# Kernel tuning notes

Hardware: AMD Instinct MI355X
Metric: run time of the kernel (lower is better)

The kernel has to match this reference:

```python
import jax, jax.numpy as jnp
import numpy as np

D_MODEL = 1024
N_HEADS = 16
D_HEAD = D_MODEL // N_HEADS
D_FF = 4 * D_MODEL
EPS = 1e-5


def _layernorm(x, g, b):
    mu = jnp.mean(x, axis=-1, keepdims=True)
    var = jnp.var(x, axis=-1, keepdims=True)
    return (x - mu) * jax.lax.rsqrt(var + EPS) * g + b


def setup_inputs() -> dict:
    key = jax.random.key(0)
    ks = jax.random.split(key, 16)
    s_attn = 1.0 / np.sqrt(D_MODEL)
    s_ff1 = 1.0 / np.sqrt(D_MODEL)
    s_ff2 = 1.0 / np.sqrt(D_FF)
    inp = {
        'x': jax.random.normal(ks[0], (2, 2048, D_MODEL), dtype=jnp.float32),
        'Wq': jax.random.uniform(ks[1], (D_MODEL, D_MODEL), jnp.float32, -s_attn, s_attn),
        'bq': jax.random.uniform(ks[2], (D_MODEL,), jnp.float32, -s_attn, s_attn),
        'Wk': jax.random.uniform(ks[3], (D_MODEL, D_MODEL), jnp.float32, -s_attn, s_attn),
        'bk': jax.random.uniform(ks[4], (D_MODEL,), jnp.float32, -s_attn, s_attn),
        'Wv': jax.random.uniform(ks[5], (D_MODEL, D_MODEL), jnp.float32, -s_attn, s_attn),
        'bv': jax.random.uniform(ks[6], (D_MODEL,), jnp.float32, -s_attn, s_attn),
        'Wo': jax.random.uniform(ks[7], (D_MODEL, D_MODEL), jnp.float32, -s_attn, s_attn),
        'bo': jax.random.uniform(ks[8], (D_MODEL,), jnp.float32, -s_attn, s_attn),
        'W1': jax.random.uniform(ks[9], (D_MODEL, D_FF), jnp.float32, -s_ff1, s_ff1),
        'b1': jax.random.uniform(ks[10], (D_FF,), jnp.float32, -s_ff1, s_ff1),
        'W2': jax.random.uniform(ks[11], (D_FF, D_MODEL), jnp.float32, -s_ff2, s_ff2),
        'b2': jax.random.uniform(ks[12], (D_MODEL,), jnp.float32, -s_ff2, s_ff2),
        'ln1_g': jnp.ones((D_MODEL,), jnp.float32),
        'ln1_b': jnp.zeros((D_MODEL,), jnp.float32),
        'ln2_g': jnp.ones((D_MODEL,), jnp.float32),
        'ln2_b': jnp.zeros((D_MODEL,), jnp.float32),
    }
    return inp


def reference(x, Wq, bq, Wk, bk, Wv, bv, Wo, bo, W1, b1, W2, b2, ln1_g, ln1_b, ln2_g, ln2_b):
    B, T, D = x.shape
    scale = D_HEAD ** -0.5

    # pre-norm MHSA + residual
    h = _layernorm(x, ln1_g, ln1_b)
    def split(z):  # [B,T,D] -> [B,H,T,d_h]
        return z.reshape(B, T, N_HEADS, D_HEAD).transpose(0, 2, 1, 3)
    Q = split(h @ Wq + bq)
    K = split(h @ Wk + bk)
    V = split(h @ Wv + bv)
    scores = jnp.einsum('bhqd,bhkd->bhqk', Q, K) * scale  # [B,H,T,T]
    attn = jax.nn.softmax(scores, axis=-1)
    out = jnp.einsum('bhqk,bhkd->bhqd', attn, V)
    out = out.transpose(0, 2, 1, 3).reshape(B, T, D)
    x = x + (out @ Wo + bo)

    # pre-norm FFN + residual
    h = _layernorm(x, ln2_g, ln2_b)
    ff = jax.nn.gelu(h @ W1 + b1, approximate=False) @ W2 + b2
    return x + ff
```

## Files before the change

### kernel.cpp

```cpp
#include <hip/hip_runtime.h>
#include <math.h>

#define SEQ   2048
#define DM    1024
#define LDQKV 3072
#define MTOK  4096

typedef float  f32x4   __attribute__((ext_vector_type(4)));
typedef __bf16 bf16x8  __attribute__((ext_vector_type(8)));
typedef short  short8  __attribute__((ext_vector_type(8)));
typedef short  short4v __attribute__((ext_vector_type(4)));

__device__ __forceinline__ short f2bf(float f) {
  union { float f; unsigned u; } v; v.f = f;
  unsigned r = v.u + 0x7fffu + ((v.u >> 16) & 1u);
  return (short)(r >> 16);
}

__device__ __forceinline__ void gl_lds16(const void* g, void* l) {
  __builtin_amdgcn_global_load_lds(
      (const __attribute__((address_space(1))) void*)g,
      (__attribute__((address_space(3))) void*)l, 16, 0, 0);
}

__device__ __forceinline__ f32x4 mfma_bf16(bf16x8 a, bf16x8 b, f32x4 c) {
  return __builtin_amdgcn_mfma_f32_16x16x32_bf16(a, b, c, 0, 0, 0);
}

__global__ __launch_bounds__(256) void transpose_cast_k(
    const float* __restrict__ W, short* __restrict__ Wt, int K, int N)
{
  __shared__ float tile[32][33];
  const int n0 = blockIdx.x * 32, k0 = blockIdx.y * 32;
  const int tx = threadIdx.x & 31, ty = threadIdx.x >> 5;
#pragma unroll
  for (int i = 0; i < 4; i++)
    tile[ty + i * 8][tx] = W[(size_t)(k0 + ty + i * 8) * N + n0 + tx];
  __syncthreads();
#pragma unroll
  for (int i = 0; i < 4; i++)
    Wt[(size_t)(n0 + ty + i * 8) * K + k0 + tx] = f2bf(tile[tx][ty + i * 8]);
}

__global__ __launch_bounds__(256) void ln_k(
    const float* __restrict__ x, const float* __restrict__ g,
    const float* __restrict__ b, short* __restrict__ out)
{
  const int row = blockIdx.x;
  const int tid = threadIdx.x;
  const float4 v = ((const float4*)(x + (size_t)row * DM))[tid];
  float s  = v.x + v.y + v.z + v.w;
  float ss = v.x * v.x + v.y * v.y + v.z * v.z + v.w * v.w;
#pragma unroll
  for (int m = 32; m >= 1; m >>= 1) { s += __shfl_xor(s, m); ss += __shfl_xor(ss, m); }
  __shared__ float red[8];
  const int wid = tid >> 6;
  if ((tid & 63) == 0) { red[wid] = s; red[4 + wid] = ss; }
  __syncthreads();
  s  = red[0] + red[1] + red[2] + red[3];
  ss = red[4] + red[5] + red[6] + red[7];
  const float mu  = s * (1.f / DM);
  const float var = ss * (1.f / DM) - mu * mu;
  const float rs  = rsqrtf(var + 1e-5f);
  const float4 gv = ((const float4*)g)[tid];
  const float4 bv = ((const float4*)b)[tid];
  short4v o;
  o[0] = f2bf((v.x - mu) * rs * gv.x + bv.x);
  o[1] = f2bf((v.y - mu) * rs * gv.y + bv.y);
  o[2] = f2bf((v.z - mu) * rs * gv.z + bv.z);
  o[3] = f2bf((v.w - mu) * rs * gv.w + bv.w);
  *(short4v*)(out + (size_t)row * DM + tid * 4) = o;
}

__global__ __launch_bounds__(256) void concat_bias_k(
    const float* __restrict__ bq, const float* __restrict__ bk,
    const float* __restrict__ bv, float* __restrict__ o)
{
  int i = blockIdx.x * 256 + threadIdx.x;
  if (i < 3072) {
    float v = (i < 1024) ? bq[i] : (i < 2048 ? bk[i - 1024] : bv[i - 2048]);
    o[i] = v;
  }
}

__global__ __launch_bounds__(256) void vtrans_k(
    const short* __restrict__ V, short* __restrict__ Vt)
{
  const int b = blockIdx.z, h = blockIdx.y, t0 = blockIdx.x * 64;
  __shared__ short tile[64][72];
  const int tid = threadIdx.x;
  const int r = tid >> 2, c = (tid & 3) * 16;
  const short* src = V + (size_t)(b * SEQ + t0 + r) * LDQKV + h * 64 + c;
  *(short8*)&tile[r][c]     = *(const short8*)src;
  *(short8*)&tile[r][c + 8] = *(const short8*)(src + 8);
  __syncthreads();
  const int d = tid >> 2;
  short8 o0, o1;
#pragma unroll
  for (int k = 0; k < 8; k++) o0[k] = tile[c + k][d];
#pragma unroll
  for (int k = 0; k < 8; k++) o1[k] = tile[c + 8 + k][d];
  short* dst = Vt + (((size_t)(b * 16 + h) * 64) + d) * 2048 + t0 + c;
  *(short8*)dst       = o0;
  *(short8*)(dst + 8) = o1;
}

template <bool GELU_, bool RESID, bool OUTBF16>
__global__ __launch_bounds__(512) void gemm256(
    const short* __restrict__ A, const short* __restrict__ Bt,
    const float* __restrict__ bias, const float* __restrict__ resid,
    void* __restrict__ Cout, int M, int N, int K)
{
  __shared__ __align__(16) short Atile[2][256 * 64];
  __shared__ __align__(16) short Btile[2][256 * 64];

  const int tid = threadIdx.x, lane = tid & 63, wid = tid >> 6;
  const int wm = wid >> 2, wn = wid & 3;

  const int nbn = N >> 8;
  const int chunk = gridDim.x >> 3;
  const int swz = (blockIdx.x & 7) * chunk + (blockIdx.x >> 3);
  const int bm = (swz / nbn) * 256;
  const int bn = (swz % nbn) * 256;

  f32x4 acc[8][4] = {};

  const int srow  = wid * 8 + (lane >> 3);
  const int sslot = (lane & 7) ^ ((lane >> 3) & 7);
  const short* Asrc = A  + (size_t)(bm + srow) * K + sslot * 8;
  const short* Bsrc = Bt + (size_t)(bn + srow) * K + sslot * 8;

#define STAGE256(buf, k0)                                                     \
  {                                                                           \
    _Pragma("unroll")                                                         \
    for (int j = 0; j < 4; j++) {                                             \
      gl_lds16(Asrc + (size_t)(j * 64) * K + (k0), &Atile[buf][(j * 64 + wid * 8) * 64]); \
      gl_lds16(Bsrc + (size_t)(j * 64) * K + (k0), &Btile[buf][(j * 64 + wid * 8) * 64]); \
    }                                                                         \
  }

  const int aRowBase = (wm * 128 + (lane & 15)) * 128;
  const int bRowBase = (wn * 64  + (lane & 15)) * 128;
  const int slot0 = (((lane >> 4)    ) ^ (lane & 7)) * 16;
  const int slot1 = (((lane >> 4) + 4) ^ (lane & 7)) * 16;

#define COMPUTE256(buf)                                                       \
  {                                                                           \
    const char* Ab_ = (const char*)&Atile[buf][0];                            \
    const char* Bb_ = (const char*)&Btile[buf][0];                            \
    _Pragma("unroll")                                                         \
    for (int ks = 0; ks < 2; ks++) {                                          \
      const int sl = ks ? slot1 : slot0;                                      \
      bf16x8 a[8], b[4];                                                      \
      _Pragma("unroll")                                                       \
      for (int mi = 0; mi < 8; mi++)                                          \
        a[mi] = *(const bf16x8*)(Ab_ + aRowBase + mi * 2048 + sl);            \
      _Pragma("unroll")                                                       \
      for (int ni = 0; ni < 4; ni++)                                          \
        b[ni] = *(const bf16x8*)(Bb_ + bRowBase + ni * 2048 + sl);            \
      __builtin_amdgcn_s_setprio(1);                                          \
      _Pragma("unroll")                                                       \
      for (int mi = 0; mi < 8; mi++)                                          \
        _Pragma("unroll")                                                     \
        for (int ni = 0; ni < 4; ni++)                                        \
          acc[mi][ni] = mfma_bf16(a[mi], b[ni], acc[mi][ni]);                 \
      __builtin_amdgcn_s_setprio(0);                                          \
    }                                                                         \
  }

  STAGE256(0, 0);
  __syncthreads();

  int cur = 0;
  const int ntiles = K >> 6;
  for (int t = 1; t < ntiles; ++t) {
    STAGE256(cur ^ 1, t * 64);
    COMPUTE256(cur);
    __syncthreads();
    cur ^= 1;
  }
  COMPUTE256(cur);

#pragma unroll
  for (int mi = 0; mi < 8; mi++) {
#pragma unroll
    for (int ni = 0; ni < 4; ni++) {
      const int col = bn + wn * 64 + ni * 16 + (lane & 15);
      const float bs = bias[col];
#pragma unroll
      for (int j = 0; j < 4; j++) {
        const int row = bm + wm * 128 + mi * 16 + (lane >> 4) * 4 + j;
        float v = acc[mi][ni][j] + bs;
        if (GELU_) v = 0.5f * v * (1.0f + erff(v * 0.70710678118654752f));
        if (RESID) v += resid[(size_t)row * N + col];
        if (OUTBF16) ((short*)Cout)[(size_t)row * N + col] = f2bf(v);
        else         ((float*)Cout)[(size_t)row * N + col] = v;
      }
    }
  }
#undef STAGE256
#undef COMPUTE256
}

template <bool GELU_, bool RESID, bool OUTBF16>
__global__ __launch_bounds__(256) void gemm_bt(
    const short* __restrict__ A, const short* __restrict__ Bt,
    const float* __restrict__ bias, const float* __restrict__ resid,
    void* __restrict__ Cout, int M, int N, int K)
{
  __shared__ __align__(16) short Abuf[2][128 * 32];
  __shared__ __align__(16) short Bbuf[2][128 * 32];
  const int tid = threadIdx.x, lane = tid & 63, wid = tid >> 6;
  const int wr = wid >> 1, wc = wid & 1;
  const int bm = blockIdx.x * 128, bn = blockIdx.y * 128;

  f32x4 acc[4][4] = {};

  const int arow  = wid * 32 + (lane >> 2);
  const int acol8 = ((lane & 3) ^ ((lane >> 2) & 3)) * 8;
  const short* Ag0 = A  + (size_t)(bm + arow)      * K + acol8;
  const short* Ag1 = A  + (size_t)(bm + arow + 16) * K + acol8;
  const short* Bg0 = Bt + (size_t)(bn + arow)      * K + acol8;
  const short* Bg1 = Bt + (size_t)(bn + arow + 16) * K + acol8;

  const int l0 = (wid * 32) * 32, l1 = (wid * 32 + 16) * 32;
  const int rslot = ((lane >> 4) ^ (lane & 3)) * 8;

  gl_lds16(Ag0, &Abuf[0][l0]);
  gl_lds16(Ag1, &Abuf[0][l1]);
  gl_lds16(Bg0, &Bbuf[0][l0]);
  gl_lds16(Bg1, &Bbuf[0][l1]);
  __syncthreads();

  int cur = 0;
  for (int k0 = 32; k0 < K; k0 += 32) {
    const int nxt = cur ^ 1;
    gl_lds16(Ag0 + k0, &Abuf[nxt][l0]);
    gl_lds16(Ag1 + k0, &Abuf[nxt][l1]);
    gl_lds16(Bg0 + k0, &Bbuf[nxt][l0]);
    gl_lds16(Bg1 + k0, &Bbuf[nxt][l1]);

    bf16x8 a[4], b[4];
#pragma unroll
    for (int mi = 0; mi < 4; mi++)
      a[mi] = *(const bf16x8*)&Abuf[cur][(wr * 64 + mi * 16 + (lane & 15)) * 32 + rslot];
#pragma unroll
    for (int ni = 0; ni < 4; ni++)
      b[ni] = *(const bf16x8*)&Bbuf[cur][(wc * 64 + ni * 16 + (lane & 15)) * 32 + rslot];
#pragma unroll
    for (int mi = 0; mi < 4; mi++)
#pragma unroll
      for (int ni = 0; ni < 4; ni++)
        acc[mi][ni] = mfma_bf16(a[mi], b[ni], acc[mi][ni]);

    __syncthreads();
    cur = nxt;
  }

  {
    bf16x8 a[4], b[4];
#pragma unroll
    for (int mi = 0; mi < 4; mi++)
      a[mi] = *(const bf16x8*)&Abuf[cur][(wr * 64 + mi * 16 + (lane & 15)) * 32 + rslot];
#pragma unroll
    for (int ni = 0; ni < 4; ni++)
      b[ni] = *(const bf16x8*)&Bbuf[cur][(wc * 64 + ni * 16 + (lane & 15)) * 32 + rslot];
#pragma unroll
    for (int mi = 0; mi < 4; mi++)
#pragma unroll
      for (int ni = 0; ni < 4; ni++)
        acc[mi][ni] = mfma_bf16(a[mi], b[ni], acc[mi][ni]);
  }

#pragma unroll
  for (int mi = 0; mi < 4; mi++) {
#pragma unroll
    for (int ni = 0; ni < 4; ni++) {
      const int col = bn + wc * 64 + ni * 16 + (lane & 15);
      const float bs = bias[col];
#pragma unroll
      for (int j = 0; j < 4; j++) {
        const int row = bm + wr * 64 + mi * 16 + (lane >> 4) * 4 + j;
        float v = acc[mi][ni][j] + bs;
        if (GELU_) v = 0.5f * v * (1.0f + erff(v * 0.70710678118654752f));
        if (RESID) v += resid[(size_t)row * N + col];
        if (OUTBF16) ((short*)Cout)[(size_t)row * N + col] = f2bf(v);
        else         ((float*)Cout)[(size_t)row * N + col] = v;
      }
    }
  }
}

template <bool GELU_, bool RESID, bool OUTBF16>
__global__ __launch_bounds__(512) void gemm_bt8(
    const short* __restrict__ A, const short* __restrict__ Bt,
    const float* __restrict__ bias, const float* __restrict__ resid,
    void* __restrict__ Cout, int M, int N, int K)
{
  __shared__ __align__(16) short Ab[2][2][128 * 32];
  __shared__ __align__(16) short Bb[2][2][64 * 32];
  const int tid = threadIdx.x, lane = tid & 63, wid = tid >> 6;
  const int kg = wid >> 2, w2 = wid & 3;
  const int wr = w2 >> 1, wc = w2 & 1;
  const int bm = blockIdx.x * 128, bn = blockIdx.y * 64;

  f32x4 acc[4][2] = {};

  const int r_l = lane >> 2;
  const int c8  = ((lane & 3) ^ ((lane >> 2) & 3)) * 8;
  const short* Ag0 = A  + (size_t)(bm + w2 * 32 + r_l)      * K + c8;
  const short* Ag1 = A  + (size_t)(bm + w2 * 32 + 16 + r_l) * K + c8;
  const short* Bg0 = Bt + (size_t)(bn + w2 * 16 + r_l)      * K + c8;

  const int la0 = (w2 * 32) * 32, la1 = (w2 * 32 + 16) * 32, lb0 = (w2 * 16) * 32;
  const int kbase = kg * 32;
  const int rslot = ((lane >> 4) ^ (lane & 3)) * 8;

  gl_lds16(Ag0 + kbase, &Ab[kg][0][la0]);
  gl_lds16(Ag1 + kbase, &Ab[kg][0][la1]);
  gl_lds16(Bg0 + kbase, &Bb[kg][0][lb0]);
  __syncthreads();

  const int nsteps = K >> 6;
  int cur = 0;
  for (int i = 1; i < nsteps; ++i) {
    const int k0 = i * 64 + kbase;
    const int nxt = cur ^ 1;
    gl_lds16(Ag0 + k0, &Ab[kg][nxt][la0]);
    gl_lds16(Ag1 + k0, &Ab[kg][nxt][la1]);
    gl_lds16(Bg0 + k0, &Bb[kg][nxt][lb0]);

    bf16x8 a[4], b[2];
#pragma unroll
    for (int mi = 0; mi < 4; mi++)
      a[mi] = *(const bf16x8*)&Ab[kg][cur][(wr * 64 + mi * 16 + (lane & 15)) * 32 + rslot];
#pragma unroll
    for (int ni = 0; ni < 2; ni++)
      b[ni] = *(const bf16x8*)&Bb[kg][cur][(wc * 32 + ni * 16 + (lane & 15)) * 32 + rslot];
#pragma unroll
    for (int mi = 0; mi < 4; mi++)
#pragma unroll
      for (int ni = 0; ni < 2; ni++)
        acc[mi][ni] = mfma_bf16(a[mi], b[ni], acc[mi][ni]);

    __syncthreads();
    cur = nxt;
  }

  {
    bf16x8 a[4], b[2];
#pragma unroll
    for (int mi = 0; mi < 4; mi++)
      a[mi] = *(const bf16x8*)&Ab[kg][cur][(wr * 64 + mi * 16 + (lane & 15)) * 32 + rslot];
#pragma unroll
    for (int ni = 0; ni < 2; ni++)
      b[ni] = *(const bf16x8*)&Bb[kg][cur][(wc * 32 + ni * 16 + (lane & 15)) * 32 + rslot];
#pragma unroll
    for (int mi = 0; mi < 4; mi++)
#pragma unroll
      for (int ni = 0; ni < 2; ni++)
        acc[mi][ni] = mfma_bf16(a[mi], b[ni], acc[mi][ni]);
  }

  __syncthreads();

  float* red = (float*)&Ab[0][0][0];
  const int slot = (w2 * 64 + lane) * 8;
  if (kg == 1) {
#pragma unroll
    for (int mi = 0; mi < 4; mi++)
#pragma unroll
      for (int ni = 0; ni < 2; ni++)
        *(f32x4*)&red[(slot + mi * 2 + ni) * 4] = acc[mi][ni];
  }
  __syncthreads();
  if (kg == 0) {
#pragma unroll
    for (int mi = 0; mi < 4; mi++)
#pragma unroll
      for (int ni = 0; ni < 2; ni++)
        acc[mi][ni] += *(const f32x4*)&red[(slot + mi * 2 + ni) * 4];

#pragma unroll
    for (int mi = 0; mi < 4; mi++) {
#pragma unroll
      for (int ni = 0; ni < 2; ni++) {
        const int col = bn + wc * 32 + ni * 16 + (lane & 15);
        const float bs = bias[col];
#pragma unroll
        for (int j = 0; j < 4; j++) {
          const int row = bm + wr * 64 + mi * 16 + (lane >> 4) * 4 + j;
          float v = acc[mi][ni][j] + bs;
          if (GELU_) v = 0.5f * v * (1.0f + erff(v * 0.70710678118654752f));
          if (RESID) v += resid[(size_t)row * N + col];
          if (OUTBF16) ((short*)Cout)[(size_t)row * N + col] = f2bf(v);
          else         ((float*)Cout)[(size_t)row * N + col] = v;
        }
      }
    }
  }
}

__global__ __launch_bounds__(512, 4) void attn_k(
    const short* __restrict__ Qg, const short* __restrict__ Kg,
    const short* __restrict__ Vt, short* __restrict__ Og)
{
  const int phys = blockIdx.x;
  const int lg = (phys & 7) * 64 + (phys >> 3);
  const int q0 = (lg & 15) * 128;
  const int h  = (lg >> 4) & 15;
  const int b  = lg >> 8;

  const int tid = threadIdx.x, lane = tid & 63, w = tid >> 6;
  const int qlane = lane & 15, g = lane >> 4;

  __shared__ __align__(16) short Kl[2][128 * 64];
  __shared__ __align__(16) short Vl[2][64 * 128];

  const size_t qrow = (size_t)(b * SEQ + q0 + w * 16 + qlane) * LDQKV + h * 64;
  const bf16x8 qf0 = *(const bf16x8*)&Qg[qrow + g * 8];
  const bf16x8 qf1 = *(const bf16x8*)&Qg[qrow + 32 + g * 8];

  const int kslot = (lane & 7) ^ ((lane >> 3) & 7);
  const short* Kg_a[2];
#pragma unroll
  for (int i = 0; i < 2; i++) {
    const int r  = i * 64 + w * 8 + (lane >> 3);
    const int kc = r >> 4, gr = (r >> 2) & 3, jr = r & 3;
    const int a  = 32 * (kc & 3) + 8 * gr + 4 * (kc >> 2) + jr;
    Kg_a[i] = Kg + ((size_t)(b * SEQ) + a) * LDQKV + h * 64 + kslot * 8;
  }
  const short* Vg_s[2];
#pragma unroll
  for (int i = 0; i < 2; i++) {
    const int d  = i * 32 + w * 4 + (lane >> 4);
    const int vs = (lane & 15) ^ (d & 15);
    Vg_s[i] = Vt + ((size_t)(b * 16 + h) * 64 + d) * 2048 + vs * 8;
  }

  float m_run = -1e30f, l_run = 0.f;
  f32x4 oacc[4] = {};
  const float C = 0.125f * 1.44269504088896f;

#pragma unroll
  for (int i = 0; i < 2; i++) {
    gl_lds16(Kg_a[i], &Kl[0][(i * 64 + w * 8) * 64]);
    gl_lds16(Vg_s[i], &Vl[0][(i * 32 + w * 4) * 128]);
  }
  __syncthreads();

  int cur = 0;
  for (int kt = 0; kt < SEQ; kt += 128) {
    const int nxt = cur ^ 1;
    if (kt + 128 < SEQ) {
#pragma unroll
      for (int i = 0; i < 2; i++) {
        gl_lds16(Kg_a[i] + (size_t)(kt + 128) * LDQKV, &Kl[nxt][(i * 64 + w * 8) * 64]);
        gl_lds16(Vg_s[i] + (kt + 128),                 &Vl[nxt][(i * 32 + w * 4) * 128]);
      }
    }
    const char* KbC = (const char*)&Kl[cur][0];
    const char* VbC = (const char*)&Vl[cur][0];

    f32x4 s[8];
#pragma unroll
    for (int kc = 0; kc < 8; kc++) {
      const int kr = kc * 16 + qlane;
      const char* kp = KbC + kr * 128;
      const int sw = (kr & 7) << 4;
      bf16x8 kf0 = *(const bf16x8*)(kp + ((g * 16) ^ sw));
      bf16x8 kf1 = *(const bf16x8*)(kp + ((64 + g * 16) ^ sw));
      f32x4 z = {};
      z = mfma_bf16(kf0, qf0, z);
      z = mfma_bf16(kf1, qf1, z);
      s[kc] = z;
    }

    f32x4 m4 = s[0];
#pragma unroll
    for (int kc = 1; kc < 8; kc++) {
      m4[0] = fmaxf(m4[0], s[kc][0]); m4[1] = fmaxf(m4[1], s[kc][1]);
      m4[2] = fmaxf(m4[2], s[kc][2]); m4[3] = fmaxf(m4[3], s[kc][3]);
    }
    float mt = fmaxf(fmaxf(m4[0], m4[1]), fmaxf(m4[2], m4[3]));
    mt = fmaxf(mt, __shfl_xor(mt, 16));
    mt = fmaxf(mt, __shfl_xor(mt, 32));

    if (!__all(mt - m_run <= 40.0f)) {
      const float mnew = fmaxf(m_run, mt);
      const float r = exp2f((m_run - mnew) * C);
      m_run = mnew;
      l_run *= r;
#pragma unroll
      for (int j = 0; j < 4; j++) {
        const float rj = __shfl(r, g * 4 + j);
#pragma unroll
        for (int dt = 0; dt < 4; dt++) oacc[dt][j] *= rj;
      }
    }

    const float nmc = -m_run * C;
    float rs = 0.f;
    unsigned pw[4][4];
#pragma unroll
    for (int kc = 0; kc < 8; kc++) {
      f32x4 p;
#pragma unroll
      for (int j = 0; j < 4; j++) p[j] = exp2f(fmaf(s[kc][j], C, nmc));
      rs += (p[0] + p[1]) + (p[2] + p[3]);
      unsigned w0, w1;
      asm("v_cvt_pk_bf16_f32 %0, %1, %2" : "=v"(w0) : "v"(p[0]), "v"(p[1]));
      asm("v_cvt_pk_bf16_f32 %0, %1, %2" : "=v"(w1) : "v"(p[2]), "v"(p[3]));
      pw[kc & 3][2 * (kc >> 2) + 0] = w0;
      pw[kc & 3][2 * (kc >> 2) + 1] = w1;
    }
    rs += __shfl_xor(rs, 16);
    rs += __shfl_xor(rs, 32);
    l_run += rs;

#pragma unroll
    for (int ks = 0; ks < 4; ks++) {
      union { unsigned u[4]; bf16x8 v; } pf;
      pf.u[0] = pw[ks][0]; pf.u[1] = pw[ks][1];
      pf.u[2] = pw[ks][2]; pf.u[3] = pw[ks][3];
#pragma unroll
      for (int dt = 0; dt < 4; dt++) {
        const int vr = dt * 16 + qlane;
        bf16x8 vf = *(const bf16x8*)(VbC + vr * 256 + ((64 * ks + 16 * g) ^ ((vr & 15) << 4)));
        oacc[dt] = mfma_bf16(pf.v, vf, oacc[dt]);
      }
    }

    __syncthreads();
    cur = nxt;
  }

  const float linv = 1.f / l_run;
#pragma unroll
  for (int j = 0; j < 4; j++) {
    const float lj = __shfl(linv, g * 4 + j);
    const int tok = q0 + w * 16 + g * 4 + j;
#pragma unroll
    for (int dt = 0; dt < 4; dt++)
      Og[(size_t)(b * SEQ + tok) * DM + h * 64 + dt * 16 + qlane] = f2bf(oacc[dt][j] * lj);
  }
}

extern "C" void kernel_launch(void* const* d_in, const int* in_sizes, int n_in,
                              void* d_out, int out_size, void* d_ws, size_t ws_size,
                              hipStream_t stream)
{
  const float* x    = (const float*)d_in[0];
  const float* Wq   = (const float*)d_in[1];
  const float* bq   = (const float*)d_in[2];
  const float* Wk   = (const float*)d_in[3];
  const float* bk   = (const float*)d_in[4];
  const float* Wv   = (const float*)d_in[5];
  const float* bv   = (const float*)d_in[6];
  const float* Wo   = (const float*)d_in[7];
  const float* bo   = (const float*)d_in[8];
  const float* W1   = (const float*)d_in[9];
  const float* b1   = (const float*)d_in[10];
  const float* W2   = (const float*)d_in[11];
  const float* b2   = (const float*)d_in[12];
  const float* ln1g = (const float*)d_in[13];
  const float* ln1b = (const float*)d_in[14];
  const float* ln2g = (const float*)d_in[15];
  const float* ln2b = (const float*)d_in[16];

  char* ws = (char*)d_ws;
  const size_t MB = 1024 * 1024;
  short* Wqkvt = (short*)(ws + 0 * MB);
  short* Wqt   = Wqkvt;
  short* Wkt   = (short*)(ws + 2 * MB);
  short* Wvt   = (short*)(ws + 4 * MB);
  short* Wot   = (short*)(ws + 6 * MB);
  short* W1t   = (short*)(ws + 8 * MB);
  short* W2t   = (short*)(ws + 16 * MB);
  short* hbuf  = (short*)(ws + 24 * MB);
  short* QKV   = (short*)(ws + 32 * MB);
  short* AO    = (short*)(ws + 56 * MB);
  float* x1    = (float*)(ws + 64 * MB);
  short* Vtb   = (short*)(ws + 64 * MB);
  float* bqkv  = (float*)(ws + 80 * MB);
  short* gbuf  = (short*)(ws + 32 * MB);

  dim3 tb(256);

  transpose_cast_k<<<dim3(32, 32),  tb, 0, stream>>>(Wq, Wqt, 1024, 1024);
  transpose_cast_k<<<dim3(32, 32),  tb, 0, stream>>>(Wk, Wkt, 1024, 1024);
  transpose_cast_k<<<dim3(32, 32),  tb, 0, stream>>>(Wv, Wvt, 1024, 1024);
  transpose_cast_k<<<dim3(32, 32),  tb, 0, stream>>>(Wo, Wot, 1024, 1024);
  transpose_cast_k<<<dim3(128, 32), tb, 0, stream>>>(W1, W1t, 1024, 4096);
  transpose_cast_k<<<dim3(32, 128), tb, 0, stream>>>(W2, W2t, 4096, 1024);
  concat_bias_k<<<dim3(12), tb, 0, stream>>>(bq, bk, bv, bqkv);

  ln_k<<<dim3(MTOK), tb, 0, stream>>>(x, ln1g, ln1b, hbuf);

  gemm_bt<false, false, true><<<dim3(32, 24), tb, 0, stream>>>(
      hbuf, Wqkvt, bqkv, nullptr, QKV, MTOK, 3072, 1024);

  vtrans_k<<<dim3(32, 16, 2), tb, 0, stream>>>(QKV + 2048, Vtb);

  attn_k<<<dim3(512), dim3(512), 0, stream>>>(QKV, QKV + 1024, Vtb, AO);

  gemm_bt8<false, true, false><<<dim3(32, 16), dim3(512), 0, stream>>>(
      AO, Wot, bo, x, x1, MTOK, 1024, 1024);

  ln_k<<<dim3(MTOK), tb, 0, stream>>>(x1, ln2g, ln2b, hbuf);

  gemm256<true, false, true><<<dim3(256), dim3(512), 0, stream>>>(
      hbuf, W1t, b1, nullptr, gbuf, MTOK, 4096, 1024);

  gemm_bt8<false, true, false><<<dim3(32, 16), dim3(512), 0, stream>>>(
      gbuf, W2t, b2, x1, (float*)d_out, MTOK, 1024, 4096);
}
```

Measured before the change: 275.1 us.

## Vectorize weight transpose-cast with 64x64 tiles and use 256-tile GEMM for QKV

Replaces the 32x32 scalar weight transpose/cast kernel with a 64x64 tile version that does float4 loads and 16-byte bf16 stores. It also switches the QKV projection from the 128x128-tile gemm_bt kernel to the larger-tile 512-thread gemm256 kernel already used for FFN1, and deletes gemm_bt. The goal is fewer memory transactions in the per-call weight conversion and more operand reuse in the QKV GEMM. The trade-off is that 192 blocks may underfill the CUs, and the tile reads with stride 65 may hit LDS bank conflicts.

Result: no change. 272.4 us (-1.0%).

```diff
diff --git a/kernel.cpp b/kernel.cpp
--- a/kernel.cpp
+++ b/kernel.cpp
@@ -27,19 +27,30 @@
   return __builtin_amdgcn_mfma_f32_16x16x32_bf16(a, b, c, 0, 0, 0);
 }
 
-__global__ __launch_bounds__(256) void transpose_cast_k(
+__global__ __launch_bounds__(256) void transpose_cast64_k(
     const float* __restrict__ W, short* __restrict__ Wt, int K, int N)
 {
-  __shared__ float tile[32][33];
-  const int n0 = blockIdx.x * 32, k0 = blockIdx.y * 32;
-  const int tx = threadIdx.x & 31, ty = threadIdx.x >> 5;
-#pragma unroll
-  for (int i = 0; i < 4; i++)
-    tile[ty + i * 8][tx] = W[(size_t)(k0 + ty + i * 8) * N + n0 + tx];
-  __syncthreads();
-#pragma unroll
-  for (int i = 0; i < 4; i++)
-    Wt[(size_t)(n0 + ty + i * 8) * K + k0 + tx] = f2bf(tile[tx][ty + i * 8]);
+  __shared__ float tile[64][65];
+  const int n0 = blockIdx.x * 64, k0 = blockIdx.y * 64;
+  const int tid = threadIdx.x;
+  const int lr = tid >> 4, lc = (tid & 15) * 4;
+#pragma unroll
+  for (int i = 0; i < 4; i++) {
+    const float4 v = *(const float4*)&W[(size_t)(k0 + lr + i * 16) * N + n0 + lc];
+    tile[lr + i * 16][lc]     = v.x;
+    tile[lr + i * 16][lc + 1] = v.y;
+    tile[lr + i * 16][lc + 2] = v.z;
+    tile[lr + i * 16][lc + 3] = v.w;
+  }
+  __syncthreads();
+  const int nr = tid >> 3, ks = (tid & 7) * 8;
+#pragma unroll
+  for (int i = 0; i < 2; i++) {
+    short8 o;
+#pragma unroll
+    for (int j = 0; j < 8; j++) o[j] = f2bf(tile[ks + j][nr + i * 32]);
+    *(short8*)&Wt[(size_t)(n0 + nr + i * 32) * K + k0 + ks] = o;
+  }
 }
 
 __global__ __launch_bounds__(256) void ln_k(
@@ -203,95 +214,6 @@
 }
 
 template <bool GELU_, bool RESID, bool OUTBF16>
-__global__ __launch_bounds__(256) void gemm_bt(
-    const short* __restrict__ A, const short* __restrict__ Bt,
-    const float* __restrict__ bias, const float* __restrict__ resid,
-    void* __restrict__ Cout, int M, int N, int K)
-{
-  __shared__ __align__(16) short Abuf[2][128 * 32];
-  __shared__ __align__(16) short Bbuf[2][128 * 32];
-  const int tid = threadIdx.x, lane = tid & 63, wid = tid >> 6;
-  const int wr = wid >> 1, wc = wid & 1;
-  const int bm = blockIdx.x * 128, bn = blockIdx.y * 128;
-
-  f32x4 acc[4][4] = {};
-
-  const int arow  = wid * 32 + (lane >> 2);
-  const int acol8 = ((lane & 3) ^ ((lane >> 2) & 3)) * 8;
-  const short* Ag0 = A  + (size_t)(bm + arow)      * K + acol8;
-  const short* Ag1 = A  + (size_t)(bm + arow + 16) * K + acol8;
-  const short* Bg0 = Bt + (size_t)(bn + arow)      * K + acol8;
-  const short* Bg1 = Bt + (size_t)(bn + arow + 16) * K + acol8;
-
-  const int l0 = (wid * 32) * 32, l1 = (wid * 32 + 16) * 32;
-  const int rslot = ((lane >> 4) ^ (lane & 3)) * 8;
-
-  gl_lds16(Ag0, &Abuf[0][l0]);
-  gl_lds16(Ag1, &Abuf[0][l1]);
-  gl_lds16(Bg0, &Bbuf[0][l0]);
-  gl_lds16(Bg1, &Bbuf[0][l1]);
-  __syncthreads();
-
-  int cur = 0;
-  for (int k0 = 32; k0 < K; k0 += 32) {
-    const int nxt = cur ^ 1;
-    gl_lds16(Ag0 + k0, &Abuf[nxt][l0]);
-    gl_lds16(Ag1 + k0, &Abuf[nxt][l1]);
-    gl_lds16(Bg0 + k0, &Bbuf[nxt][l0]);
-    gl_lds16(Bg1 + k0, &Bbuf[nxt][l1]);
-
-    bf16x8 a[4], b[4];
-#pragma unroll
-    for (int mi = 0; mi < 4; mi++)
-      a[mi] = *(const bf16x8*)&Abuf[cur][(wr * 64 + mi * 16 + (lane & 15)) * 32 + rslot];
-#pragma unroll
-    for (int ni = 0; ni < 4; ni++)
-      b[ni] = *(const bf16x8*)&Bbuf[cur][(wc * 64 + ni * 16 + (lane & 15)) * 32 + rslot];
-#pragma unroll
-    for (int mi = 0; mi < 4; mi++)
-#pragma unroll
-      for (int ni = 0; ni < 4; ni++)
-        acc[mi][ni] = mfma_bf16(a[mi], b[ni], acc[mi][ni]);
-
-    __syncthreads();
-    cur = nxt;
-  }
-
-  {
-    bf16x8 a[4], b[4];
-#pragma unroll
-    for (int mi = 0; mi < 4; mi++)
-      a[mi] = *(const bf16x8*)&Abuf[cur][(wr * 64 + mi * 16 + (lane & 15)) * 32 + rslot];
-#pragma unroll
-    for (int ni = 0; ni < 4; ni++)
-      b[ni] = *(const bf16x8*)&Bbuf[cur][(wc * 64 + ni * 16 + (lane & 15)) * 32 + rslot];
-#pragma unroll
-    for (int mi = 0; mi < 4; mi++)
-#pragma unroll
-      for (int ni = 0; ni < 4; ni++)
-        acc[mi][ni] = mfma_bf16(a[mi], b[ni], acc[mi][ni]);
-  }
-
-#pragma unroll
-  for (int mi = 0; mi < 4; mi++) {
-#pragma unroll
-    for (int ni = 0; ni < 4; ni++) {
-      const int col = bn + wc * 64 + ni * 16 + (lane & 15);
-      const float bs = bias[col];
-#pragma unroll
-      for (int j = 0; j < 4; j++) {
-        const int row = bm + wr * 64 + mi * 16 + (lane >> 4) * 4 + j;
-        float v = acc[mi][ni][j] + bs;
-        if (GELU_) v = 0.5f * v * (1.0f + erff(v * 0.70710678118654752f));
-        if (RESID) v += resid[(size_t)row * N + col];
-        if (OUTBF16) ((short*)Cout)[(size_t)row * N + col] = f2bf(v);
-        else         ((float*)Cout)[(size_t)row * N + col] = v;
-      }
-    }
-  }
-}
-
-template <bool GELU_, bool RESID, bool OUTBF16>
 __global__ __launch_bounds__(512) void gemm_bt8(
     const short* __restrict__ A, const short* __restrict__ Bt,
     const float* __restrict__ bias, const float* __restrict__ resid,
@@ -587,17 +509,17 @@
 
   dim3 tb(256);
 
-  transpose_cast_k<<<dim3(32, 32),  tb, 0, stream>>>(Wq, Wqt, 1024, 1024);
-  transpose_cast_k<<<dim3(32, 32),  tb, 0, stream>>>(Wk, Wkt, 1024, 1024);
-  transpose_cast_k<<<dim3(32, 32),  tb, 0, stream>>>(Wv, Wvt, 1024, 1024);
-  transpose_cast_k<<<dim3(32, 32),  tb, 0, stream>>>(Wo, Wot, 1024, 1024);
-  transpose_cast_k<<<dim3(128, 32), tb, 0, stream>>>(W1, W1t, 1024, 4096);
-  transpose_cast_k<<<dim3(32, 128), tb, 0, stream>>>(W2, W2t, 4096, 1024);
+  transpose_cast64_k<<<dim3(16, 16), tb, 0, stream>>>(Wq, Wqt, 1024, 1024);
+  transpose_cast64_k<<<dim3(16, 16), tb, 0, stream>>>(Wk, Wkt, 1024, 1024);
+  transpose_cast64_k<<<dim3(16, 16), tb, 0, stream>>>(Wv, Wvt, 1024, 1024);
+  transpose_cast64_k<<<dim3(16, 16), tb, 0, stream>>>(Wo, Wot, 1024, 1024);
+  transpose_cast64_k<<<dim3(64, 16), tb, 0, stream>>>(W1, W1t, 1024, 4096);
+  transpose_cast64_k<<<dim3(16, 64), tb, 0, stream>>>(W2, W2t, 4096, 1024);
   concat_bias_k<<<dim3(12), tb, 0, stream>>>(bq, bk, bv, bqkv);
 
   ln_k<<<dim3(MTOK), tb, 0, stream>>>(x, ln1g, ln1b, hbuf);
 
-  gemm_bt<false, false, true><<<dim3(32, 24), tb, 0, stream>>>(
+  gemm256<false, false, true><<<dim3(192), dim3(512), 0, stream>>>(
       hbuf, Wqkvt, bqkv, nullptr, QKV, MTOK, 3072, 1024);
 
   vtrans_k<<<dim3(32, 16, 2), tb, 0, stream>>>(QKV + 2048, Vtb);
```
